# Kernel tuning notes

Hardware: AMD Instinct MI355X
Metric: run time of the kernel (lower is better)

Reference implementation:

```python
import jax, jax.numpy as jnp
import numpy as np

NUM_HEADS = 8
DIM = 256
SCALE = (DIM // NUM_HEADS) ** -0.5  # head_dim = dim // nhead = 32


def setup_inputs() -> dict:
    key = jax.random.key(0)
    k1, k2, k3, k4, k5 = jax.random.split(key, 5)
    B, N = 1, 4096
    qk = jax.random.normal(k1, (B, N, 3 * DIM), dtype=jnp.float32)
    v_cls = jax.random.normal(k2, (B, N, 2 * DIM), dtype=jnp.float32)
    masks = jax.random.uniform(k3, (B, N, N), dtype=jnp.float32)
    # torch Linear weights stored as [in, out] for x @ W
    W_qk = jax.random.normal(k4, (3 * DIM, 6 * DIM), dtype=jnp.float32) * (3 * DIM) ** -0.5
    W_v = jax.random.normal(k5, (2 * DIM, 2 * DIM), dtype=jnp.float32) * (2 * DIM) ** -0.5
    return {"qk": qk, "v_cls": v_cls, "masks": masks, "W_qk": W_qk, "W_v": W_v}


def reference(qk, v_cls, masks, W_qk, W_v):
    B, N, C_qk = qk.shape
    C_cls = v_cls.shape[-1]
    H = NUM_HEADS
    hd_qk = C_qk // H   # 96
    hd_v = C_cls // H   # 64

    # qk projection: [B,N,6*dim] -> (2,B,H,N,hd_qk)
    proj = (qk @ W_qk).reshape(B, N, 2, H, hd_qk).transpose(2, 0, 3, 1, 4)
    q, k = proj[0], proj[1]                      # [B,H,N,hd_qk]
    v = (v_cls @ W_v).reshape(B, N, H, hd_v).transpose(0, 2, 1, 3)  # [B,H,N,hd_v]

    attn = jnp.einsum('bhnd,bhmd->bhnm', q, k) * SCALE
    attn = jax.nn.softmax(attn, axis=-1)

    # post-softmax mask-mul and renorm by mask-sum and head count
    m = masks[:, None]                           # [B,1,N,N] broadcast over heads
    attn = attn * m / (H * jnp.sum(m, axis=-1, keepdims=True))
    # attn_drop with p=0.0 is identity in eval

    x_cls = jnp.einsum('bhnm,bhmd->bhnd', attn, v)
    return x_cls.transpose(0, 2, 1, 3).reshape(B, N, C_cls)
```

## Files before the change

### kernel.cpp

```cpp
#include <hip/hip_runtime.h>

typedef __attribute__((ext_vector_type(8))) _Float16 half8;
typedef __attribute__((ext_vector_type(4))) _Float16 half4;
typedef __attribute__((ext_vector_type(4))) float f32x4;

#define N_SEQ 4096
#define HD_QK 96
#define HD_V  64
#define NHEADS 8
#define QSCALE 0.25505545556f
#define ESHIFT 8.0f

__global__ __launch_bounds__(256) void cast_f16(const float* __restrict__ in,
                                                _Float16* __restrict__ out) {
    size_t i = ((size_t)blockIdx.x * 256 + threadIdx.x) * 8;
    float4 a = *(const float4*)(in + i);
    float4 b = *(const float4*)(in + i + 4);
    half8 h;
    h[0] = (_Float16)a.x; h[1] = (_Float16)a.y; h[2] = (_Float16)a.z; h[3] = (_Float16)a.w;
    h[4] = (_Float16)b.x; h[5] = (_Float16)b.y; h[6] = (_Float16)b.z; h[7] = (_Float16)b.w;
    *(half8*)(out + i) = h;
}

__global__ __launch_bounds__(256) void transpose_cast(const float* __restrict__ in,
                                                      _Float16* __restrict__ out,
                                                      int R, int C) {
    __shared__ float tile[32][33];
    int tx = threadIdx.x & 31, ty = threadIdx.x >> 5;
    int c0 = blockIdx.x * 32, r0 = blockIdx.y * 32;
    for (int k = 0; k < 4; k++)
        tile[ty + 8 * k][tx] = in[(size_t)(r0 + ty + 8 * k) * C + c0 + tx];
    __syncthreads();
    for (int k = 0; k < 4; k++)
        out[(size_t)(c0 + ty + 8 * k) * R + r0 + tx] = (_Float16)tile[tx][ty + 8 * k];
}

__global__ __launch_bounds__(256) void proj_gemm(
    const _Float16* __restrict__ X, const _Float16* __restrict__ Wt,
    _Float16* __restrict__ Qh, _Float16* __restrict__ Kh,
    _Float16* __restrict__ Vtg, int K, int mode)
{
    __shared__ _Float16 smem[2][128][72];

    const int t = threadIdx.x;
    const int lane = t & 63, wv = t >> 6;
    const int quad = lane >> 4, l15 = lane & 15;
    const int n0 = blockIdx.x * 128, row0 = blockIdx.y * 128;
    const int mB = (wv & 1) * 64, nB = (wv >> 1) * 64;
    const int sr = t >> 1, sk = (t & 1) * 32;

    const f32x4 fzero = {0.f, 0.f, 0.f, 0.f};
    f32x4 acc[4][4];
    for (int i = 0; i < 4; i++)
        for (int j = 0; j < 4; j++) acc[i][j] = fzero;

    for (int k0 = 0; k0 < K; k0 += 64) {
        __syncthreads();
        {
            const _Float16* xp = X + (size_t)(row0 + sr) * K + k0 + sk;
            *(half8*)&smem[0][sr][sk]      = *(const half8*)xp;
            *(half8*)&smem[0][sr][sk + 8]  = *(const half8*)(xp + 8);
            *(half8*)&smem[0][sr][sk + 16] = *(const half8*)(xp + 16);
            *(half8*)&smem[0][sr][sk + 24] = *(const half8*)(xp + 24);
            const _Float16* wp = Wt + (size_t)(n0 + sr) * K + k0 + sk;
            *(half8*)&smem[1][sr][sk]      = *(const half8*)wp;
            *(half8*)&smem[1][sr][sk + 8]  = *(const half8*)(wp + 8);
            *(half8*)&smem[1][sr][sk + 16] = *(const half8*)(wp + 16);
            *(half8*)&smem[1][sr][sk + 24] = *(const half8*)(wp + 24);
        }
        __syncthreads();
        for (int c = 0; c < 2; c++) {
            half8 a[4], b[4];
            for (int i = 0; i < 4; i++)
                a[i] = *(const half8*)&smem[0][mB + 16 * i + l15][c * 32 + quad * 8];
            for (int j = 0; j < 4; j++)
                b[j] = *(const half8*)&smem[1][nB + 16 * j + l15][c * 32 + quad * 8];
            for (int i = 0; i < 4; i++)
                for (int j = 0; j < 4; j++)
                    acc[i][j] = __builtin_amdgcn_mfma_f32_16x16x32_f16(a[i], b[j], acc[i][j], 0, 0, 0);
        }
    }

    __syncthreads();
    _Float16 (*Ct)[136] = (_Float16 (*)[136])smem;
    for (int j = 0; j < 4; j++) {
        int col = n0 + nB + 16 * j + l15;
        float scl = (mode == 0 && col < 768) ? QSCALE : 1.0f;
        for (int i = 0; i < 4; i++)
            for (int r = 0; r < 4; r++)
                Ct[mB + 16 * i + quad * 4 + r][nB + 16 * j + l15] =
                    (_Float16)(acc[i][j][r] * scl);
    }
    __syncthreads();

    if (mode == 0) {
        for (int e = 0; e < 8; e++) {
            int id = e * 256 + t;
            int row = id >> 4, cc = id & 15;
            int col = n0 + cc * 8;
            int w = col >= 768 ? 1 : 0;
            int rem = col - w * 768;
            int h = rem / 96, d = rem - h * 96;
            _Float16* dst = w ? Kh : Qh;
            half8 v = *(const half8*)&Ct[row][cc * 8];
            *(half8*)&dst[((size_t)h * N_SEQ + row0 + row) * HD_QK + d] = v;
        }
    } else {
        for (int e = 0; e < 4; e++) {
            int id = e * 256 + t;
            int col = id >> 3, rc = id & 7;
            int c = n0 + col;
            int h = c >> 6, d = c & 63;
            half8 v0, v1;
            for (int k = 0; k < 8; k++) {
                v0[k] = Ct[rc * 16 + k][col];
                v1[k] = Ct[rc * 16 + 8 + k][col];
            }
            _Float16* dst = &Vtg[((size_t)h * HD_V + d) * N_SEQ + row0 + rc * 16];
            *(half8*)dst = v0;
            *(half8*)(dst + 8) = v1;
        }
    }
}

__global__ __launch_bounds__(256, 2) void flash_attn(
    const _Float16* __restrict__ Qh, const _Float16* __restrict__ Kh,
    const _Float16* __restrict__ Vtg, const float* __restrict__ masks,
    float* __restrict__ out)
{
    __shared__ __align__(16) float Obuf[4][64][68];
    __shared__ float Lbuf[4][64];
    __shared__ float Mbuf[4][64];

    const int t = threadIdx.x;
    const int lane = t & 63, w = t >> 6;
    const int quad = lane >> 4, l15 = lane & 15;
    const int head = blockIdx.y;
    const int q0 = blockIdx.x * 64;

    half8 qf[3][4];
    for (int nt = 0; nt < 4; nt++) {
        const _Float16* qp = Qh + ((size_t)head * N_SEQ + q0 + 16 * nt + l15) * HD_QK + 8 * quad;
        for (int c = 0; c < 3; c++)
            qf[c][nt] = *(const half8*)(qp + 32 * c);
    }

    const _Float16* kbase = Kh + ((size_t)head * N_SEQ + 16 * w + l15) * HD_QK + 8 * quad;
    const _Float16* vbase = Vtg + ((size_t)head * HD_V + l15) * N_SEQ + 16 * w + 4 * quad;
    const float*    mbase = masks + (size_t)(q0 + l15) * N_SEQ + 16 * w + 4 * quad;

    const f32x4 fzero = {0.f, 0.f, 0.f, 0.f};
    f32x4 oacc[4][4];
    for (int nt = 0; nt < 4; nt++)
        for (int v = 0; v < 4; v++) oacc[nt][v] = fzero;
    float lsum[4] = {0.f, 0.f, 0.f, 0.f};
    float msum[4] = {0.f, 0.f, 0.f, 0.f};

    half8 kf[2][3];
    half4 vf[2][4];
    float4 mf[2][4];
    for (int c = 0; c < 3; c++) kf[0][c] = *(const half8*)(kbase + 32 * c);
    for (int v = 0; v < 4; v++) vf[0][v] = *(const half4*)(vbase + (size_t)(16 * v) * N_SEQ);
    for (int nt = 0; nt < 4; nt++) mf[0][nt] = *(const float4*)(mbase + (size_t)(16 * nt) * N_SEQ);

#pragma unroll 2
    for (int kb = 0; kb < 64; kb++) {
        const int cu = kb & 1, nx = cu ^ 1;
        {
            int kn = kb < 63 ? kb + 1 : 63;
            const _Float16* kp = kbase + (size_t)kn * 64 * HD_QK;
            for (int c = 0; c < 3; c++) kf[nx][c] = *(const half8*)(kp + 32 * c);
            const _Float16* vp = vbase + kn * 64;
            for (int v = 0; v < 4; v++) vf[nx][v] = *(const half4*)(vp + (size_t)(16 * v) * N_SEQ);
            const float* mp = mbase + kn * 64;
            for (int nt = 0; nt < 4; nt++) mf[nx][nt] = *(const float4*)(mp + (size_t)(16 * nt) * N_SEQ);
        }

        f32x4 sT[4];
        for (int nt = 0; nt < 4; nt++) sT[nt] = fzero;
        for (int c = 0; c < 3; c++)
            for (int nt = 0; nt < 4; nt++)
                sT[nt] = __builtin_amdgcn_mfma_f32_16x16x32_f16(kf[cu][c], qf[c][nt], sT[nt], 0, 0, 0);

        half4 af[4];
        for (int nt = 0; nt < 4; nt++) {
            float4 mv = mf[cu][nt];
            float p0 = exp2f(sT[nt][0] - ESHIFT);
            float p1 = exp2f(sT[nt][1] - ESHIFT);
            float p2 = exp2f(sT[nt][2] - ESHIFT);
            float p3 = exp2f(sT[nt][3] - ESHIFT);
            lsum[nt] += (p0 + p1) + (p2 + p3);
            msum[nt] += (mv.x + mv.y) + (mv.z + mv.w);
            half4 a;
            a[0] = (_Float16)(p0 * mv.x);
            a[1] = (_Float16)(p1 * mv.y);
            a[2] = (_Float16)(p2 * mv.z);
            a[3] = (_Float16)(p3 * mv.w);
            af[nt] = a;
        }

        for (int nt = 0; nt < 4; nt++)
            for (int v = 0; v < 4; v++)
                oacc[nt][v] = __builtin_amdgcn_mfma_f32_16x16x16f16(af[nt], vf[cu][v], oacc[nt][v], 0, 0, 0);
    }

    for (int nt = 0; nt < 4; nt++) {
        lsum[nt] += __shfl_xor(lsum[nt], 16);
        lsum[nt] += __shfl_xor(lsum[nt], 32);
        msum[nt] += __shfl_xor(msum[nt], 16);
        msum[nt] += __shfl_xor(msum[nt], 32);
        if (quad == 0) {
            Lbuf[w][16 * nt + l15] = lsum[nt];
            Mbuf[w][16 * nt + l15] = msum[nt];
        }
        for (int v = 0; v < 4; v++)
            for (int r = 0; r < 4; r++)
                Obuf[w][16 * nt + 4 * quad + r][16 * v + l15] = oacc[nt][v][r];
    }
    __syncthreads();

    {
        int r = t >> 2;
        int dc = (t & 3) * 16;
        float lt = Lbuf[0][r] + Lbuf[1][r] + Lbuf[2][r] + Lbuf[3][r];
        float mt = Mbuf[0][r] + Mbuf[1][r] + Mbuf[2][r] + Mbuf[3][r];
        float inv = 1.0f / (lt * (float)NHEADS * mt);
        for (int g = 0; g < 4; g++) {
            f32x4 s = *(const f32x4*)&Obuf[0][r][dc + 4 * g];
            s += *(const f32x4*)&Obuf[1][r][dc + 4 * g];
            s += *(const f32x4*)&Obuf[2][r][dc + 4 * g];
            s += *(const f32x4*)&Obuf[3][r][dc + 4 * g];
            s *= inv;
            *(f32x4*)&out[(size_t)(q0 + r) * (NHEADS * HD_V) + head * HD_V + dc + 4 * g] = s;
        }
    }
}

extern "C" void kernel_launch(void* const* d_in, const int* in_sizes, int n_in,
                              void* d_out, int out_size, void* d_ws, size_t ws_size,
                              hipStream_t stream) {
    const float* qk    = (const float*)d_in[0];
    const float* v_cls = (const float*)d_in[1];
    const float* masks = (const float*)d_in[2];
    const float* W_qk  = (const float*)d_in[3];
    const float* W_v   = (const float*)d_in[4];
    float* out = (float*)d_out;

    char* wsp = (char*)d_ws;
    size_t off = 0;
    auto alloc = [&](size_t elems) { _Float16* p = (_Float16*)(wsp + off); off += elems * 2; return p; };
    _Float16* Xh   = alloc((size_t)N_SEQ * 768);
    _Float16* Vch  = alloc((size_t)N_SEQ * 512);
    _Float16* Wqkt = alloc((size_t)1536 * 768);
    _Float16* Wvt  = alloc((size_t)512 * 512);
    _Float16* Qh   = alloc((size_t)NHEADS * N_SEQ * HD_QK);
    _Float16* Kh   = alloc((size_t)NHEADS * N_SEQ * HD_QK);
    _Float16* Vtg  = alloc((size_t)NHEADS * HD_V * N_SEQ);
    (void)ws_size;

    dim3 blk(256);
    cast_f16<<<dim3((N_SEQ * 768) / (8 * 256)), blk, 0, stream>>>(qk, Xh);
    cast_f16<<<dim3((N_SEQ * 512) / (8 * 256)), blk, 0, stream>>>(v_cls, Vch);
    transpose_cast<<<dim3(1536 / 32, 768 / 32), blk, 0, stream>>>(W_qk, Wqkt, 768, 1536);
    transpose_cast<<<dim3(512 / 32, 512 / 32), blk, 0, stream>>>(W_v, Wvt, 512, 512);

    proj_gemm<<<dim3(1536 / 128, N_SEQ / 128), blk, 0, stream>>>(
        Xh, Wqkt, Qh, Kh, Vtg, 768, 0);
    proj_gemm<<<dim3(512 / 128, N_SEQ / 128), blk, 0, stream>>>(
        Vch, Wvt, Qh, Kh, Vtg, 512, 1);

    flash_attn<<<dim3(N_SEQ / 64, NHEADS), blk, 0, stream>>>(
        Qh, Kh, Vtg, masks, out);
}
```

Measured before the change: 296.3 us.

## Split attention over key range, fuse input casts into projection GEMM

```diff
diff --git a/kernel.cpp b/kernel.cpp
--- a/kernel.cpp
+++ b/kernel.cpp
@@ -11,15 +11,11 @@
 #define QSCALE 0.25505545556f
 #define ESHIFT 8.0f
 
-__global__ __launch_bounds__(256) void cast_f16(const float* __restrict__ in,
-                                                _Float16* __restrict__ out) {
-    size_t i = ((size_t)blockIdx.x * 256 + threadIdx.x) * 8;
-    float4 a = *(const float4*)(in + i);
-    float4 b = *(const float4*)(in + i + 4);
+__device__ inline half8 cvt8(float4 a, float4 b) {
     half8 h;
     h[0] = (_Float16)a.x; h[1] = (_Float16)a.y; h[2] = (_Float16)a.z; h[3] = (_Float16)a.w;
     h[4] = (_Float16)b.x; h[5] = (_Float16)b.y; h[6] = (_Float16)b.z; h[7] = (_Float16)b.w;
-    *(half8*)(out + i) = h;
+    return h;
 }
 
 __global__ __launch_bounds__(256) void transpose_cast(const float* __restrict__ in,
@@ -35,49 +31,63 @@
         out[(size_t)(c0 + ty + 8 * k) * R + r0 + tx] = (_Float16)tile[tx][ty + 8 * k];
 }
 
-__global__ __launch_bounds__(256) void proj_gemm(
-    const _Float16* __restrict__ X, const _Float16* __restrict__ Wt,
+__global__ __launch_bounds__(256) void proj_fused(
+    const float* __restrict__ Xqk, const float* __restrict__ Xv,
+    const _Float16* __restrict__ Wqkt, const _Float16* __restrict__ Wvt,
     _Float16* __restrict__ Qh, _Float16* __restrict__ Kh,
-    _Float16* __restrict__ Vtg, int K, int mode)
+    _Float16* __restrict__ Vtg)
 {
-    __shared__ _Float16 smem[2][128][72];
+    __shared__ _Float16 smem[64 * 72 + 128 * 72];
+    _Float16 (*Xs)[72] = (_Float16 (*)[72])smem;
+    _Float16 (*Ws)[72] = (_Float16 (*)[72])(smem + 64 * 72);
 
     const int t = threadIdx.x;
     const int lane = t & 63, wv = t >> 6;
     const int quad = lane >> 4, l15 = lane & 15;
-    const int n0 = blockIdx.x * 128, row0 = blockIdx.y * 128;
-    const int mB = (wv & 1) * 64, nB = (wv >> 1) * 64;
-    const int sr = t >> 1, sk = (t & 1) * 32;
+    const bool qkmode = blockIdx.x < 12;
+    const int n0 = qkmode ? blockIdx.x * 128 : (blockIdx.x - 12) * 128;
+    const int row0 = blockIdx.y * 64;
+    const int K = qkmode ? 768 : 512;
+    const float* X = qkmode ? Xqk : Xv;
+    const _Float16* Wt = qkmode ? Wqkt : Wvt;
+
+    const int mB = (wv & 1) * 32, nB = (wv >> 1) * 64;
+    const int xr = t >> 2, xc = (t & 3) * 16;
+    const int wr = t >> 1, wc = (t & 1) * 32;
 
     const f32x4 fzero = {0.f, 0.f, 0.f, 0.f};
-    f32x4 acc[4][4];
-    for (int i = 0; i < 4; i++)
+    f32x4 acc[2][4];
+    for (int i = 0; i < 2; i++)
         for (int j = 0; j < 4; j++) acc[i][j] = fzero;
 
     for (int k0 = 0; k0 < K; k0 += 64) {
         __syncthreads();
         {
-            const _Float16* xp = X + (size_t)(row0 + sr) * K + k0 + sk;
-            *(half8*)&smem[0][sr][sk]      = *(const half8*)xp;
-            *(half8*)&smem[0][sr][sk + 8]  = *(const half8*)(xp + 8);
-            *(half8*)&smem[0][sr][sk + 16] = *(const half8*)(xp + 16);
-            *(half8*)&smem[0][sr][sk + 24] = *(const half8*)(xp + 24);
-            const _Float16* wp = Wt + (size_t)(n0 + sr) * K + k0 + sk;
-            *(half8*)&smem[1][sr][sk]      = *(const half8*)wp;
-            *(half8*)&smem[1][sr][sk + 8]  = *(const half8*)(wp + 8);
-            *(half8*)&smem[1][sr][sk + 16] = *(const half8*)(wp + 16);
-            *(half8*)&smem[1][sr][sk + 24] = *(const half8*)(wp + 24);
+            const float* xp = X + (size_t)(row0 + xr) * K + k0 + xc;
+            float4 a0 = *(const float4*)xp;
+            float4 a1 = *(const float4*)(xp + 4);
+            float4 a2 = *(const float4*)(xp + 8);
+            float4 a3 = *(const float4*)(xp + 12);
+            *(half8*)&Xs[xr][xc]     = cvt8(a0, a1);
+            *(half8*)&Xs[xr][xc + 8] = cvt8(a2, a3);
+        }
+        {
+            const _Float16* wp = Wt + (size_t)(n0 + wr) * K + k0 + wc;
+            *(half8*)&Ws[wr][wc]      = *(const half8*)wp;
+            *(half8*)&Ws[wr][wc + 8]  = *(const half8*)(wp + 8);
+            *(half8*)&Ws[wr][wc + 16] = *(const half8*)(wp + 16);
+            *(half8*)&Ws[wr][wc + 24] = *(const half8*)(wp + 24);
         }
         __syncthreads();
         for (int c = 0; c < 2; c++) {
-            half8 a[4], b[4];
-            for (int i = 0; i < 4; i++)
-                a[i] = *(const half8*)&smem[0][mB + 16 * i + l15][c * 32 + quad * 8];
+            half8 af[2], bf[4];
+            for (int i = 0; i < 2; i++)
+                af[i] = *(const half8*)&Xs[mB + 16 * i + l15][c * 32 + quad * 8];
             for (int j = 0; j < 4; j++)
-                b[j] = *(const half8*)&smem[1][nB + 16 * j + l15][c * 32 + quad * 8];
-            for (int i = 0; i < 4; i++)
+                bf[j] = *(const half8*)&Ws[nB + 16 * j + l15][c * 32 + quad * 8];
+            for (int i = 0; i < 2; i++)
                 for (int j = 0; j < 4; j++)
-                    acc[i][j] = __builtin_amdgcn_mfma_f32_16x16x32_f16(a[i], b[j], acc[i][j], 0, 0, 0);
+                    acc[i][j] = __builtin_amdgcn_mfma_f32_16x16x32_f16(af[i], bf[j], acc[i][j], 0, 0, 0);
         }
     }
 
@@ -85,16 +95,16 @@
     _Float16 (*Ct)[136] = (_Float16 (*)[136])smem;
     for (int j = 0; j < 4; j++) {
         int col = n0 + nB + 16 * j + l15;
-        float scl = (mode == 0 && col < 768) ? QSCALE : 1.0f;
-        for (int i = 0; i < 4; i++)
+        float scl = (qkmode && col < 768) ? QSCALE : 1.0f;
+        for (int i = 0; i < 2; i++)
             for (int r = 0; r < 4; r++)
                 Ct[mB + 16 * i + quad * 4 + r][nB + 16 * j + l15] =
                     (_Float16)(acc[i][j][r] * scl);
     }
     __syncthreads();
 
-    if (mode == 0) {
-        for (int e = 0; e < 8; e++) {
+    if (qkmode) {
+        for (int e = 0; e < 4; e++) {
             int id = e * 256 + t;
             int row = id >> 4, cc = id & 15;
             int col = n0 + cc * 8;
@@ -102,13 +112,13 @@
             int rem = col - w * 768;
             int h = rem / 96, d = rem - h * 96;
             _Float16* dst = w ? Kh : Qh;
-            half8 v = *(const half8*)&Ct[row][cc * 8];
-            *(half8*)&dst[((size_t)h * N_SEQ + row0 + row) * HD_QK + d] = v;
+            *(half8*)&dst[((size_t)h * N_SEQ + row0 + row) * HD_QK + d] =
+                *(const half8*)&Ct[row][cc * 8];
         }
     } else {
-        for (int e = 0; e < 4; e++) {
+        for (int e = 0; e < 2; e++) {
             int id = e * 256 + t;
-            int col = id >> 3, rc = id & 7;
+            int col = id >> 2, rc = id & 3;
             int c = n0 + col;
             int h = c >> 6, d = c & 63;
             half8 v0, v1;
@@ -123,20 +133,22 @@
     }
 }
 
-__global__ __launch_bounds__(256, 2) void flash_attn(
+__global__ __launch_bounds__(256, 4) void flash_attn(
     const _Float16* __restrict__ Qh, const _Float16* __restrict__ Kh,
     const _Float16* __restrict__ Vtg, const float* __restrict__ masks,
-    float* __restrict__ out)
+    float* __restrict__ Ows, float* __restrict__ Lws, float* __restrict__ Mws)
 {
-    __shared__ __align__(16) float Obuf[4][64][68];
-    __shared__ float Lbuf[4][64];
-    __shared__ float Mbuf[4][64];
+    __shared__ __align__(16) float Ob[2][64][68];
+    __shared__ float Lb[2][64];
+    __shared__ float Mb[2][64];
 
     const int t = threadIdx.x;
     const int lane = t & 63, w = t >> 6;
     const int quad = lane >> 4, l15 = lane & 15;
     const int head = blockIdx.y;
     const int q0 = blockIdx.x * 64;
+    const int z = blockIdx.z;
+    const int kb0 = z * 32, kbE = kb0 + 32;
 
     half8 qf[3][4];
     for (int nt = 0; nt < 4; nt++) {
@@ -159,15 +171,15 @@
     half8 kf[2][3];
     half4 vf[2][4];
     float4 mf[2][4];
-    for (int c = 0; c < 3; c++) kf[0][c] = *(const half8*)(kbase + 32 * c);
-    for (int v = 0; v < 4; v++) vf[0][v] = *(const half4*)(vbase + (size_t)(16 * v) * N_SEQ);
-    for (int nt = 0; nt < 4; nt++) mf[0][nt] = *(const float4*)(mbase + (size_t)(16 * nt) * N_SEQ);
+    for (int c = 0; c < 3; c++) kf[0][c] = *(const half8*)(kbase + (size_t)kb0 * 64 * HD_QK + 32 * c);
+    for (int v = 0; v < 4; v++) vf[0][v] = *(const half4*)(vbase + (size_t)(16 * v) * N_SEQ + kb0 * 64);
+    for (int nt = 0; nt < 4; nt++) mf[0][nt] = *(const float4*)(mbase + (size_t)(16 * nt) * N_SEQ + kb0 * 64);
 
 #pragma unroll 2
-    for (int kb = 0; kb < 64; kb++) {
+    for (int kb = kb0; kb < kbE; kb++) {
         const int cu = kb & 1, nx = cu ^ 1;
         {
-            int kn = kb < 63 ? kb + 1 : 63;
+            int kn = (kb + 1 < kbE) ? kb + 1 : kb;
             const _Float16* kp = kbase + (size_t)kn * 64 * HD_QK;
             for (int c = 0; c < 3; c++) kf[nx][c] = *(const half8*)(kp + 32 * c);
             const _Float16* vp = vbase + kn * 64;
@@ -209,31 +221,60 @@
         lsum[nt] += __shfl_xor(lsum[nt], 32);
         msum[nt] += __shfl_xor(msum[nt], 16);
         msum[nt] += __shfl_xor(msum[nt], 32);
-        if (quad == 0) {
-            Lbuf[w][16 * nt + l15] = lsum[nt];
-            Mbuf[w][16 * nt + l15] = msum[nt];
-        }
-        for (int v = 0; v < 4; v++)
-            for (int r = 0; r < 4; r++)
-                Obuf[w][16 * nt + 4 * quad + r][16 * v + l15] = oacc[nt][v][r];
+    }
+
+    if (w & 1) {
+        for (int nt = 0; nt < 4; nt++) {
+            for (int v = 0; v < 4; v++)
+                for (int r = 0; r < 4; r++)
+                    Ob[w >> 1][16 * nt + 4 * quad + r][16 * v + l15] = oacc[nt][v][r];
+            if (quad == 0) {
+                Lb[w >> 1][16 * nt + l15] = lsum[nt];
+                Mb[w >> 1][16 * nt + l15] = msum[nt];
+            }
+        }
+    }
+    __syncthreads();
+    if (!(w & 1)) {
+        for (int nt = 0; nt < 4; nt++) {
+            for (int v = 0; v < 4; v++)
+                for (int r = 0; r < 4; r++)
+                    Ob[w >> 1][16 * nt + 4 * quad + r][16 * v + l15] += oacc[nt][v][r];
+            if (quad == 0) {
+                Lb[w >> 1][16 * nt + l15] += lsum[nt];
+                Mb[w >> 1][16 * nt + l15] += msum[nt];
+            }
+        }
     }
     __syncthreads();
 
     {
-        int r = t >> 2;
-        int dc = (t & 3) * 16;
-        float lt = Lbuf[0][r] + Lbuf[1][r] + Lbuf[2][r] + Lbuf[3][r];
-        float mt = Mbuf[0][r] + Mbuf[1][r] + Mbuf[2][r] + Mbuf[3][r];
-        float inv = 1.0f / (lt * (float)NHEADS * mt);
+        int row = t >> 2, c0 = (t & 3) * 16;
+        float* obase = Ows + (size_t)z * N_SEQ * 512 + (size_t)(q0 + row) * 512 + head * HD_V + c0;
         for (int g = 0; g < 4; g++) {
-            f32x4 s = *(const f32x4*)&Obuf[0][r][dc + 4 * g];
-            s += *(const f32x4*)&Obuf[1][r][dc + 4 * g];
-            s += *(const f32x4*)&Obuf[2][r][dc + 4 * g];
-            s += *(const f32x4*)&Obuf[3][r][dc + 4 * g];
-            s *= inv;
-            *(f32x4*)&out[(size_t)(q0 + r) * (NHEADS * HD_V) + head * HD_V + dc + 4 * g] = s;
-        }
-    }
+            f32x4 s = *(const f32x4*)&Ob[0][row][c0 + 4 * g];
+            s += *(const f32x4*)&Ob[1][row][c0 + 4 * g];
+            *(f32x4*)(obase + 4 * g) = s;
+        }
+        if (t < 64)
+            Lws[(size_t)z * NHEADS * N_SEQ + head * N_SEQ + q0 + t] = Lb[0][t] + Lb[1][t];
+        else if (t < 128)
+            Mws[(size_t)z * NHEADS * N_SEQ + head * N_SEQ + q0 + (t - 64)] = Mb[0][t - 64] + Mb[1][t - 64];
+    }
+}
+
+__global__ __launch_bounds__(256) void finalize(
+    const float* __restrict__ Ows, const float* __restrict__ Lws,
+    const float* __restrict__ Mws, float* __restrict__ out)
+{
+    size_t o = ((size_t)blockIdx.x * 256 + threadIdx.x) * 4;
+    int q = (int)(o >> 9);
+    int head = (int)((o & 511) >> 6);
+    f32x4 a = *(const f32x4*)(Ows + o);
+    a += *(const f32x4*)(Ows + (size_t)N_SEQ * 512 + o);
+    float l = Lws[head * N_SEQ + q] + Lws[NHEADS * N_SEQ + head * N_SEQ + q];
+    float m = Mws[head * N_SEQ + q] + Mws[NHEADS * N_SEQ + head * N_SEQ + q];
+    *(f32x4*)(out + o) = a * (1.0f / (l * (float)NHEADS * m));
 }
 
 extern "C" void kernel_launch(void* const* d_in, const int* in_sizes, int n_in,
@@ -248,27 +289,28 @@
 
     char* wsp = (char*)d_ws;
     size_t off = 0;
-    auto alloc = [&](size_t elems) { _Float16* p = (_Float16*)(wsp + off); off += elems * 2; return p; };
-    _Float16* Xh   = alloc((size_t)N_SEQ * 768);
-    _Float16* Vch  = alloc((size_t)N_SEQ * 512);
-    _Float16* Wqkt = alloc((size_t)1536 * 768);
-    _Float16* Wvt  = alloc((size_t)512 * 512);
-    _Float16* Qh   = alloc((size_t)NHEADS * N_SEQ * HD_QK);
-    _Float16* Kh   = alloc((size_t)NHEADS * N_SEQ * HD_QK);
-    _Float16* Vtg  = alloc((size_t)NHEADS * HD_V * N_SEQ);
+    auto allocH = [&](size_t elems) { _Float16* p = (_Float16*)(wsp + off); off += elems * 2; return p; };
+    _Float16* Wqkt = allocH((size_t)1536 * 768);
+    _Float16* Wvt  = allocH((size_t)512 * 512);
+    _Float16* Qh   = allocH((size_t)NHEADS * N_SEQ * HD_QK);
+    _Float16* Kh   = allocH((size_t)NHEADS * N_SEQ * HD_QK);
+    _Float16* Vtg  = allocH((size_t)NHEADS * HD_V * N_SEQ);
+    auto allocF = [&](size_t elems) { float* p = (float*)(wsp + off); off += elems * 4; return p; };
+    float* Ows = allocF((size_t)2 * N_SEQ * 512);
+    float* Lws = allocF((size_t)2 * NHEADS * N_SEQ);
+    float* Mws = allocF((size_t)2 * NHEADS * N_SEQ);
     (void)ws_size;
 
     dim3 blk(256);
-    cast_f16<<<dim3((N_SEQ * 768) / (8 * 256)), blk, 0, stream>>>(qk, Xh);
-    cast_f16<<<dim3((N_SEQ * 512) / (8 * 256)), blk, 0, stream>>>(v_cls, Vch);
     transpose_cast<<<dim3(1536 / 32, 768 / 32), blk, 0, stream>>>(W_qk, Wqkt, 768, 1536);
     transpose_cast<<<dim3(512 / 32, 512 / 32), blk, 0, stream>>>(W_v, Wvt, 512, 512);
 
-    proj_gemm<<<dim3(1536 / 128, N_SEQ / 128), blk, 0, stream>>>(
-        Xh, Wqkt, Qh, Kh, Vtg, 768, 0);
-    proj_gemm<<<dim3(512 / 128, N_SEQ / 128), blk, 0, stream>>>(
-        Vch, Wvt, Qh, Kh, Vtg, 512, 1);
-
-    flash_attn<<<dim3(N_SEQ / 64, NHEADS), blk, 0, stream>>>(
-        Qh, Kh, Vtg, masks, out);
-}
+    proj_fused<<<dim3(16, N_SEQ / 64), blk, 0, stream>>>(
+        qk, v_cls, Wqkt, Wvt, Qh, Kh, Vtg);
+
+    flash_attn<<<dim3(N_SEQ / 64, NHEADS, 2), blk, 0, stream>>>(
+        Qh, Kh, Vtg, masks, Ows, Lws, Mws);
+
+    finalize<<<dim3((N_SEQ * 512) / (256 * 4)), blk, 0, stream>>>(
+        Ows, Lws, Mws, out);
+}
```

New measurement: 614.6 us. +107.4%, slower.
